# Optimization experiments

Measured on AMD Instinct MI355X. Metric: run time of the kernel, lower is better.

The kernel has to match this reference:

```python
import jax, jax.numpy as jnp
import numpy as np

D, DK, DV = 1024, 128, 128
N = 8192


def setup_inputs() -> dict:
    key = jax.random.key(0)
    ks = jax.random.split(key, 7)
    s = 1.0 / np.sqrt(D)
    return {
        "X": jax.random.normal(ks[0], (N, D), dtype=jnp.float32),
        "Wq": jax.random.uniform(ks[1], (D, DK), jnp.float32, -s, s),
        "bq": jax.random.uniform(ks[2], (DK,), jnp.float32, -s, s),
        "Wk": jax.random.uniform(ks[3], (D, DK), jnp.float32, -s, s),
        "bk": jax.random.uniform(ks[4], (DK,), jnp.float32, -s, s),
        "Wv": jax.random.uniform(ks[5], (D, DV), jnp.float32, -s, s),
        "bv": jax.random.uniform(ks[6], (DV,), jnp.float32, -s, s),
    }


def reference(X, Wq, bq, Wk, bk, Wv, bv):
    # Projections (torch Linear: y = x @ W^T + b; here W stored as [in, out])
    Q = X @ Wq + bq            # [N, d_k]
    K = X @ Wk + bk            # [N, d_k]
    V = X @ Wv + bv            # [N, d_v]
    n, d_k = Q.shape
    scores = (Q @ K.T) / jnp.sqrt(jnp.asarray(d_k, Q.dtype))  # [N, N]
    # Causal mask: positions j > i get -inf before softmax
    causal = jnp.tril(jnp.ones((n, n), dtype=bool))
    scores = jnp.where(causal, scores, -jnp.inf)
    weights = jax.nn.softmax(scores, axis=-1)  # [N, N]
    return weights @ V          # [N, d_v]
```

## Files before the change

kernel.cpp:

```cpp
#include <hip/hip_runtime.h>
#include <hip/hip_bf16.h>

#define N_TOK 8192
#define D_IN  1024
#define DK    128
#define NT    256

typedef __attribute__((ext_vector_type(8))) short short8;
typedef __attribute__((ext_vector_type(4))) float f32x4;

static __device__ __forceinline__ unsigned short f2bf(float f) {
    __hip_bfloat16 h = __float2bfloat16(f);
    return __builtin_bit_cast(unsigned short, h);
}

static __device__ __forceinline__ void gl_lds16(const void* g, void* l) {
    __builtin_amdgcn_global_load_lds(
        (const __attribute__((address_space(1))) void*)g,
        (__attribute__((address_space(3))) void*)l, 16, 0, 0);
}

__global__ __launch_bounds__(256) void wtrans_kernel(
    const float* __restrict__ Wq, const float* __restrict__ Wk,
    const float* __restrict__ Wv, unsigned short* __restrict__ Wt)
{
    __shared__ unsigned short T[64][72];
    const int proj = blockIdx.y;
    const float* W = (proj == 0) ? Wq : (proj == 1) ? Wk : Wv;
    unsigned short* out = Wt + (size_t)proj * DK * D_IN;
    const int k0 = (blockIdx.x & 15) * 64, n0 = (blockIdx.x >> 4) * 64;
    const int tid = threadIdx.x;
    #pragma unroll
    for (int i = 0; i < 4; i++) {
        int e = tid + i * 256;
        int r = e >> 4, c4 = e & 15;
        float4 v = *reinterpret_cast<const float4*>(&W[(size_t)(k0 + r) * DK + n0 + c4 * 4]);
        T[c4 * 4 + 0][r] = f2bf(v.x);
        T[c4 * 4 + 1][r] = f2bf(v.y);
        T[c4 * 4 + 2][r] = f2bf(v.z);
        T[c4 * 4 + 3][r] = f2bf(v.w);
    }
    __syncthreads();
    #pragma unroll
    for (int i = 0; i < 4; i++) {
        int e = tid + i * 256;
        int r = e >> 4, c4 = e & 15;
        *reinterpret_cast<ushort4*>(&out[(size_t)(n0 + r) * D_IN + k0 + c4 * 4]) =
            *reinterpret_cast<const ushort4*>(&T[r][c4 * 4]);
    }
}

__global__ __launch_bounds__(256) void proj_fused(
    const float* __restrict__ X, const unsigned short* __restrict__ Wt,
    const float* __restrict__ bq, const float* __restrict__ bk,
    const float* __restrict__ bv,
    unsigned short* __restrict__ Qb, unsigned short* __restrict__ Kb,
    unsigned short* __restrict__ Vt)
{
    __shared__ unsigned short Xs[2][32][72];

    const int tid = threadIdx.x;
    const int wid = tid >> 6, lane = tid & 63;
    const int g = lane >> 4, r16 = lane & 15;
    const int mb = blockIdx.x * 32;

    float4 xr[2];
    auto XLOAD = [&](int k0) {
        #pragma unroll
        for (int i = 0; i < 2; i++) {
            int e = tid + i * 256;
            int r = e >> 4, c4 = e & 15;
            xr[i] = *reinterpret_cast<const float4*>(
                &X[(size_t)(mb + r) * D_IN + k0 + c4 * 4]);
        }
    };
    auto XWRITE = [&](int buf) {
        #pragma unroll
        for (int i = 0; i < 2; i++) {
            int e = tid + i * 256;
            int r = e >> 4, c4 = e & 15;
            ushort4 h;
            h.x = f2bf(xr[i].x); h.y = f2bf(xr[i].y);
            h.z = f2bf(xr[i].z); h.w = f2bf(xr[i].w);
            *reinterpret_cast<ushort4*>(&Xs[buf][r][c4 * 4]) = h;
        }
    };

    f32x4 acc[2][6] = {};

    XLOAD(0); XWRITE(0);
    __syncthreads();
    for (int s = 0; s < 16; ++s) {
        const int k0 = s * 64;
        const int cur = s & 1;
        if (s + 1 < 16) XLOAD(k0 + 64);
        #pragma unroll
        for (int kk = 0; kk < 64; kk += 32) {
            short8 af[2], bfr[6];
            #pragma unroll
            for (int mi = 0; mi < 2; mi++)
                af[mi] = *reinterpret_cast<const short8*>(&Xs[cur][mi * 16 + r16][kk + g * 8]);
            #pragma unroll
            for (int ni = 0; ni < 6; ni++) {
                int nn = wid * 96 + ni * 16;
                int pj = nn >> 7;
                bfr[ni] = *reinterpret_cast<const short8*>(
                    &Wt[((size_t)pj * DK + (nn & 127) + r16) * D_IN + k0 + kk + g * 8]);
            }
            __builtin_amdgcn_s_setprio(1);
            #pragma unroll
            for (int mi = 0; mi < 2; mi++)
                #pragma unroll
                for (int ni = 0; ni < 6; ni++)
                    acc[mi][ni] = __builtin_amdgcn_mfma_f32_16x16x32_bf16(
                        af[mi], bfr[ni], acc[mi][ni], 0, 0, 0);
            __builtin_amdgcn_s_setprio(0);
        }
        if (s + 1 < 16) XWRITE((s + 1) & 1);
        __syncthreads();
    }

    #pragma unroll
    for (int ni = 0; ni < 6; ni++) {
        int nn = wid * 96 + ni * 16;
        int pj = nn >> 7;
        int n = (nn & 127) + r16;
        const float* bias = (pj == 0) ? bq : (pj == 1) ? bk : bv;
        float b = bias[n];
        if (pj < 2) {
            unsigned short* out = (pj == 0) ? Qb : Kb;
            #pragma unroll
            for (int mi = 0; mi < 2; mi++)
                #pragma unroll
                for (int e = 0; e < 4; e++) {
                    int m = mb + mi * 16 + g * 4 + e;
                    int nc = n;
                    if (pj == 1)
                        nc = ((((n >> 3) ^ (m & 7)) << 3) | (n & 7));
                    out[(size_t)m * DK + nc] = f2bf(acc[mi][ni][e] + b);
                }
        } else {
            #pragma unroll
            for (int mi = 0; mi < 2; mi++) {
                int m0 = mb + mi * 16 + g * 4;
                int mblk = (((m0 & 31) >> 3) ^ (n & 3));
                int mp = (m0 & ~31) | (mblk << 3) | (m0 & 7);
                ushort4 h;
                h.x = f2bf(acc[mi][ni][0] + b);
                h.y = f2bf(acc[mi][ni][1] + b);
                h.z = f2bf(acc[mi][ni][2] + b);
                h.w = f2bf(acc[mi][ni][3] + b);
                *reinterpret_cast<ushort4*>(&Vt[(size_t)n * N_TOK + mp]) = h;
            }
        }
    }
}

__global__ __launch_bounds__(256, 3) void attn_partial(
    const unsigned short* __restrict__ Qb, const unsigned short* __restrict__ Ksw,
    const unsigned short* __restrict__ Vsw,
    float* __restrict__ Opart, float* __restrict__ Mpart, float* __restrict__ Lpart,
    float* __restrict__ O, int chunk_tiles, int max_chunks, int direct)
{
    __shared__ unsigned short Klds[2][32][128];
    __shared__ unsigned short Vlds[2][128][32];
    __shared__ unsigned short Pq[4][32][36];

    const int qb = blockIdx.x, c = blockIdx.y;
    const int j0 = c * chunk_tiles;
    const int jmax = 4 * qb + 4;
    const int jend = min(j0 + chunk_tiles, jmax);
    if (j0 >= jend) return;
    const int nt = jend - j0;

    const int tid = threadIdx.x;
    const int wid = tid >> 6, lane = tid & 63;
    const int g = lane >> 4, r16 = lane & 15;
    const int t = qb * 4 + wid;
    const int qw = t * 32;
    const float scale2 = 0.08838834764831845f * 1.4426950408889634f;

    auto STAGE = [&](int buf, int kvb) {
        #pragma unroll
        for (int s = 0; s < 2; s++) {
            int ob = ((wid * 2 + s) << 10);
            gl_lds16((const char*)Ksw + ((size_t)kvb << 8) + ob + (lane << 4),
                     (char*)&Klds[buf][0][0] + ob);
        }
        #pragma unroll
        for (int s = 0; s < 2; s++) {
            int ob = ((wid * 2 + s) << 10);
            int o = ob + (lane << 4);
            int d = o >> 6, cb = o & 63;
            gl_lds16((const char*)Vsw + (((size_t)d * N_TOK + kvb) << 1) + cb,
                     (char*)&Vlds[buf][0][0] + ob);
        }
    };

    short8 qf[2][4];
    #pragma unroll
    for (int mi = 0; mi < 2; mi++)
        #pragma unroll
        for (int kd = 0; kd < 4; kd++)
            qf[mi][kd] = *reinterpret_cast<const short8*>(
                &Qb[(size_t)(qw + mi * 16 + r16) * DK + kd * 32 + g * 8]);

    f32x4 o_acc[2][8] = {};
    float m_run[2] = {-1e30f, -1e30f}, l_run[2] = {0.f, 0.f};

    STAGE(0, j0 * 32);

    int cur = 0;
    for (int it = 0; it < nt; ++it) {
        const int kvb = (j0 + it) * 32;
        if (it + 1 < nt) {
            STAGE(cur ^ 1, kvb + 32);
            asm volatile("s_waitcnt vmcnt(4)" ::: "memory");
        } else {
            asm volatile("s_waitcnt vmcnt(0)" ::: "memory");
        }
        __builtin_amdgcn_sched_barrier(0);
        __builtin_amdgcn_s_barrier();
        __builtin_amdgcn_sched_barrier(0);

        const unsigned short* Kl = &Klds[cur][0][0];
        const unsigned short* Vl = &Vlds[cur][0][0];

        f32x4 st[2][2] = {};
        #pragma unroll
        for (int kd = 0; kd < 4; kd++) {
            int swb = ((((kd << 2) | g) ^ (r16 & 7)) << 3);
            short8 kf0 = *reinterpret_cast<const short8*>(Kl + r16 * 128 + swb);
            short8 kf1 = *reinterpret_cast<const short8*>(Kl + (16 + r16) * 128 + swb);
            __builtin_amdgcn_s_setprio(1);
            st[0][0] = __builtin_amdgcn_mfma_f32_16x16x32_bf16(kf0, qf[0][kd], st[0][0], 0, 0, 0);
            st[0][1] = __builtin_amdgcn_mfma_f32_16x16x32_bf16(kf0, qf[1][kd], st[0][1], 0, 0, 0);
            st[1][0] = __builtin_amdgcn_mfma_f32_16x16x32_bf16(kf1, qf[0][kd], st[1][0], 0, 0, 0);
            st[1][1] = __builtin_amdgcn_mfma_f32_16x16x32_bf16(kf1, qf[1][kd], st[1][1], 0, 0, 0);
            __builtin_amdgcn_s_setprio(0);
        }

        const bool anymask = (kvb + 31 > qw);
        float alpha[2];
        #pragma unroll
        for (int mi = 0; mi < 2; mi++) {
            const int qrow = qw + mi * 16 + r16;
            float s[2][4];
            #pragma unroll
            for (int ni = 0; ni < 2; ni++)
                #pragma unroll
                for (int e = 0; e < 4; e++) {
                    float v = st[ni][mi][e] * scale2;
                    if (anymask && (kvb + ni * 16 + g * 4 + e > qrow)) v = -1e30f;
                    s[ni][e] = v;
                }
            float lm = fmaxf(fmaxf(fmaxf(s[0][0], s[0][1]), fmaxf(s[0][2], s[0][3])),
                             fmaxf(fmaxf(s[1][0], s[1][1]), fmaxf(s[1][2], s[1][3])));
            lm = fmaxf(lm, __shfl_xor(lm, 16));
            lm = fmaxf(lm, __shfl_xor(lm, 32));
            float mnew = fmaxf(m_run[mi], lm);
            alpha[mi] = exp2f(m_run[mi] - mnew);
            float ps[2][4], ls;
            #pragma unroll
            for (int ni = 0; ni < 2; ni++)
                #pragma unroll
                for (int e = 0; e < 4; e++)
                    ps[ni][e] = exp2f(s[ni][e] - mnew);
            ls = ((ps[0][0] + ps[0][1]) + (ps[0][2] + ps[0][3]))
               + ((ps[1][0] + ps[1][1]) + (ps[1][2] + ps[1][3]));
            ls += __shfl_xor(ls, 16);
            ls += __shfl_xor(ls, 32);
            l_run[mi] = l_run[mi] * alpha[mi] + ls;
            m_run[mi] = mnew;
            #pragma unroll
            for (int ni = 0; ni < 2; ni++) {
                ushort4 pk;
                pk.x = f2bf(ps[ni][0]); pk.y = f2bf(ps[ni][1]);
                pk.z = f2bf(ps[ni][2]); pk.w = f2bf(ps[ni][3]);
                *reinterpret_cast<ushort4*>(&Pq[wid][mi * 16 + r16][ni * 16 + g * 4]) = pk;
            }
        }
        if (__any(alpha[0] < 1.f) || __any(alpha[1] < 1.f)) {
            #pragma unroll
            for (int mi = 0; mi < 2; mi++)
                #pragma unroll
                for (int df = 0; df < 8; df++)
                    #pragma unroll
                    for (int e = 0; e < 4; e++)
                        o_acc[mi][df][e] *= alpha[mi];
        }
        short8 pb0 = *reinterpret_cast<const short8*>(&Pq[wid][r16][g * 8]);
        short8 pb1 = *reinterpret_cast<const short8*>(&Pq[wid][16 + r16][g * 8]);
        const int swv = ((g ^ (r16 & 3)) << 3);
        #pragma unroll
        for (int df = 0; df < 8; df++) {
            short8 vf = *reinterpret_cast<const short8*>(Vl + (df * 16 + r16) * 32 + swv);
            __builtin_amdgcn_s_setprio(1);
            o_acc[0][df] = __builtin_amdgcn_mfma_f32_16x16x32_bf16(vf, pb0, o_acc[0][df], 0, 0, 0);
            o_acc[1][df] = __builtin_amdgcn_mfma_f32_16x16x32_bf16(vf, pb1, o_acc[1][df], 0, 0, 0);
            __builtin_amdgcn_s_setprio(0);
        }

        __builtin_amdgcn_sched_barrier(0);
        __builtin_amdgcn_s_barrier();
        __builtin_amdgcn_sched_barrier(0);
        cur ^= 1;
    }

    if (direct) {
        #pragma unroll
        for (int mi = 0; mi < 2; mi++) {
            float inv = 1.0f / l_run[mi];
            #pragma unroll
            for (int df = 0; df < 8; df++) {
                f32x4 r = o_acc[mi][df];
                r[0] *= inv; r[1] *= inv; r[2] *= inv; r[3] *= inv;
                *reinterpret_cast<f32x4*>(
                    &O[(size_t)(qw + mi * 16 + r16) * DK + df * 16 + g * 4]) = r;
            }
        }
    } else {
        size_t pb0i = ((size_t)t * max_chunks + c) * 32;
        #pragma unroll
        for (int mi = 0; mi < 2; mi++) {
            #pragma unroll
            for (int df = 0; df < 8; df++)
                *reinterpret_cast<f32x4*>(
                    &Opart[(pb0i + mi * 16 + r16) * 128 + df * 16 + g * 4]) = o_acc[mi][df];
            if (g == 0) {
                Mpart[pb0i + mi * 16 + r16] = m_run[mi];
                Lpart[pb0i + mi * 16 + r16] = l_run[mi];
            }
        }
    }
}

__global__ __launch_bounds__(256) void attn_merge(
    const float* __restrict__ Opart, const float* __restrict__ Mpart,
    const float* __restrict__ Lpart, float* __restrict__ O,
    int chunk_tiles, int max_chunks)
{
    __shared__ float Ms[32], Ls[32], Fs[16][32];
    const int t = blockIdx.x;
    const int nc = t / chunk_tiles + 1;
    const int tid = threadIdx.x;

    if (tid < 32) {
        float M = -1e30f;
        for (int c = 0; c < nc; c++)
            M = fmaxf(M, Mpart[((size_t)t * max_chunks + c) * 32 + tid]);
        float L = 0.f;
        for (int c = 0; c < nc; c++) {
            size_t pb = ((size_t)t * max_chunks + c) * 32 + tid;
            L += exp2f(Mpart[pb] - M) * Lpart[pb];
        }
        Ms[tid] = M; Ls[tid] = L;
    }
    __syncthreads();
    for (int cc = tid >> 5; cc < nc; cc += 8) {
        int row = tid & 31;
        Fs[cc][row] = exp2f(Mpart[((size_t)t * max_chunks + cc) * 32 + row] - Ms[row]);
    }
    __syncthreads();
    #pragma unroll
    for (int it = 0; it < 4; it++) {
        int idx = tid + it * 256;
        int row = idx >> 5, c4 = idx & 31;
        float4 acc = {0.f, 0.f, 0.f, 0.f};
        for (int c = 0; c < nc; c++) {
            const float4 v = *reinterpret_cast<const float4*>(
                &Opart[(((size_t)t * max_chunks + c) * 32 + row) * 128 + c4 * 4]);
            float f = Fs[c][row];
            acc.x += f * v.x; acc.y += f * v.y; acc.z += f * v.z; acc.w += f * v.w;
        }
        float inv = 1.0f / Ls[row];
        float4 r;
        r.x = acc.x * inv; r.y = acc.y * inv; r.z = acc.z * inv; r.w = acc.w * inv;
        *reinterpret_cast<float4*>(&O[((size_t)t * 32 + row) * DK + c4 * 4]) = r;
    }
}

extern "C" void kernel_launch(void* const* d_in, const int* in_sizes, int n_in,
                              void* d_out, int out_size, void* d_ws, size_t ws_size,
                              hipStream_t stream) {
    const float* X  = (const float*)d_in[0];
    const float* Wq = (const float*)d_in[1];
    const float* bq = (const float*)d_in[2];
    const float* Wk = (const float*)d_in[3];
    const float* bk = (const float*)d_in[4];
    const float* Wv = (const float*)d_in[5];
    const float* bv = (const float*)d_in[6];
    float* O = (float*)d_out;

    unsigned short* Qb = (unsigned short*)d_ws;
    unsigned short* Kb = Qb + (size_t)N_TOK * DK;
    unsigned short* Vt = Kb + (size_t)N_TOK * DK;
    unsigned short* Wt = Vt + (size_t)N_TOK * DK;
    float* Opart = (float*)(Wt + (size_t)3 * DK * D_IN);
    size_t base_bytes = (size_t)((char*)Opart - (char*)d_ws);

    int chunk_tiles = 0, max_chunks = 1, direct = 0;
    const int opts[4] = {16, 32, 64, 128};
    for (int i = 0; i < 4; i++) {
        int ct = opts[i], mc = NT / ct;
        size_t need = base_bytes + (size_t)NT * mc * 32 * (128 + 2) * sizeof(float);
        if (need <= ws_size) { chunk_tiles = ct; max_chunks = mc; break; }
    }
    if (!chunk_tiles) { chunk_tiles = NT; max_chunks = 1; direct = 1; }
    float* Mpart = Opart + (size_t)NT * max_chunks * 32 * 128;
    float* Lpart = Mpart + (size_t)NT * max_chunks * 32;

    wtrans_kernel<<<dim3(32, 3), 256, 0, stream>>>(Wq, Wk, Wv, Wt);
    proj_fused<<<dim3(256), 256, 0, stream>>>(X, Wt, bq, bk, bv, Qb, Kb, Vt);
    int grid_c = direct ? 1 : max_chunks;
    attn_partial<<<dim3(64, grid_c), 256, 0, stream>>>(
        Qb, Kb, Vt, Opart, Mpart, Lpart, O, chunk_tiles, max_chunks, direct);
    if (!direct)
        attn_merge<<<dim3(NT), 256, 0, stream>>>(Opart, Mpart, Lpart, O,
                                                 chunk_tiles, max_chunks);
}
```

Measured before the change: 112.4 us.

## Split projection grid, lazy softmax rescale, register P shuffle, bf16 partial outputs

The projection kernel now launches twice as many blocks, each covering half the output columns. The attention kernel gets a tighter occupancy bound and skips the online-softmax max update and accumulator rescale while the new row max exceeds the running max by at most 8. It builds the P operand with packed bf16 converts and cross-lane shuffles instead of a round trip through LDS. Partial outputs are stored as bf16 rather than fp32, which halves merge traffic and permits a smaller chunk size of 8, at the cost of extra rounding error in the merged result.

```diff
diff --git a/kernel.cpp b/kernel.cpp
--- a/kernel.cpp
+++ b/kernel.cpp
@@ -62,7 +62,8 @@
     const int tid = threadIdx.x;
     const int wid = tid >> 6, lane = tid & 63;
     const int g = lane >> 4, r16 = lane & 15;
-    const int mb = blockIdx.x * 32;
+    const int mb   = (blockIdx.x >> 1) * 32;
+    const int half = blockIdx.x & 1;
 
     float4 xr[2];
     auto XLOAD = [&](int k0) {
@@ -86,7 +87,7 @@
         }
     };
 
-    f32x4 acc[2][6] = {};
+    f32x4 acc[2][3] = {};
 
     XLOAD(0); XWRITE(0);
     __syncthreads();
@@ -96,13 +97,13 @@
         if (s + 1 < 16) XLOAD(k0 + 64);
         #pragma unroll
         for (int kk = 0; kk < 64; kk += 32) {
-            short8 af[2], bfr[6];
+            short8 af[2], bfr[3];
             #pragma unroll
             for (int mi = 0; mi < 2; mi++)
                 af[mi] = *reinterpret_cast<const short8*>(&Xs[cur][mi * 16 + r16][kk + g * 8]);
             #pragma unroll
-            for (int ni = 0; ni < 6; ni++) {
-                int nn = wid * 96 + ni * 16;
+            for (int ni = 0; ni < 3; ni++) {
+                int nn = half * 192 + wid * 48 + ni * 16;
                 int pj = nn >> 7;
                 bfr[ni] = *reinterpret_cast<const short8*>(
                     &Wt[((size_t)pj * DK + (nn & 127) + r16) * D_IN + k0 + kk + g * 8]);
@@ -111,7 +112,7 @@
             #pragma unroll
             for (int mi = 0; mi < 2; mi++)
                 #pragma unroll
-                for (int ni = 0; ni < 6; ni++)
+                for (int ni = 0; ni < 3; ni++)
                     acc[mi][ni] = __builtin_amdgcn_mfma_f32_16x16x32_bf16(
                         af[mi], bfr[ni], acc[mi][ni], 0, 0, 0);
             __builtin_amdgcn_s_setprio(0);
@@ -121,8 +122,8 @@
     }
 
     #pragma unroll
-    for (int ni = 0; ni < 6; ni++) {
-        int nn = wid * 96 + ni * 16;
+    for (int ni = 0; ni < 3; ni++) {
+        int nn = half * 192 + wid * 48 + ni * 16;
         int pj = nn >> 7;
         int n = (nn & 127) + r16;
         const float* bias = (pj == 0) ? bq : (pj == 1) ? bk : bv;
@@ -156,15 +157,15 @@
     }
 }
 
-__global__ __launch_bounds__(256, 3) void attn_partial(
+__global__ __launch_bounds__(256, 4) void attn_partial(
     const unsigned short* __restrict__ Qb, const unsigned short* __restrict__ Ksw,
     const unsigned short* __restrict__ Vsw,
-    float* __restrict__ Opart, float* __restrict__ Mpart, float* __restrict__ Lpart,
+    unsigned short* __restrict__ OpartH, float* __restrict__ Mpart,
+    float* __restrict__ Lpart,
     float* __restrict__ O, int chunk_tiles, int max_chunks, int direct)
 {
     __shared__ unsigned short Klds[2][32][128];
     __shared__ unsigned short Vlds[2][128][32];
-    __shared__ unsigned short Pq[4][32][36];
 
     const int qb = blockIdx.x, c = blockIdx.y;
     const int j0 = c * chunk_tiles;
@@ -241,7 +242,7 @@
         }
 
         const bool anymask = (kvb + 31 > qw);
-        float alpha[2];
+        short8 pb[2];
         #pragma unroll
         for (int mi = 0; mi < 2; mi++) {
             const int qrow = qw + mi * 16 + r16;
@@ -258,46 +259,54 @@
                              fmaxf(fmaxf(s[1][0], s[1][1]), fmaxf(s[1][2], s[1][3])));
             lm = fmaxf(lm, __shfl_xor(lm, 16));
             lm = fmaxf(lm, __shfl_xor(lm, 32));
-            float mnew = fmaxf(m_run[mi], lm);
-            alpha[mi] = exp2f(m_run[mi] - mnew);
-            float ps[2][4], ls;
+            bool nog = __all(lm - m_run[mi] <= 8.0f);
+            float mnew = nog ? m_run[mi] : fmaxf(m_run[mi], lm);
+            float ps[2][4];
             #pragma unroll
             for (int ni = 0; ni < 2; ni++)
                 #pragma unroll
                 for (int e = 0; e < 4; e++)
                     ps[ni][e] = exp2f(s[ni][e] - mnew);
-            ls = ((ps[0][0] + ps[0][1]) + (ps[0][2] + ps[0][3]))
-               + ((ps[1][0] + ps[1][1]) + (ps[1][2] + ps[1][3]));
+            float ls = ((ps[0][0] + ps[0][1]) + (ps[0][2] + ps[0][3]))
+                     + ((ps[1][0] + ps[1][1]) + (ps[1][2] + ps[1][3]));
             ls += __shfl_xor(ls, 16);
             ls += __shfl_xor(ls, 32);
-            l_run[mi] = l_run[mi] * alpha[mi] + ls;
-            m_run[mi] = mnew;
-            #pragma unroll
-            for (int ni = 0; ni < 2; ni++) {
-                ushort4 pk;
-                pk.x = f2bf(ps[ni][0]); pk.y = f2bf(ps[ni][1]);
-                pk.z = f2bf(ps[ni][2]); pk.w = f2bf(ps[ni][3]);
-                *reinterpret_cast<ushort4*>(&Pq[wid][mi * 16 + r16][ni * 16 + g * 4]) = pk;
-            }
-        }
-        if (__any(alpha[0] < 1.f) || __any(alpha[1] < 1.f)) {
-            #pragma unroll
-            for (int mi = 0; mi < 2; mi++)
+            if (nog) {
+                l_run[mi] += ls;
+            } else {
+                float alpha = exp2f(m_run[mi] - mnew);
+                l_run[mi] = l_run[mi] * alpha + ls;
+                m_run[mi] = mnew;
                 #pragma unroll
                 for (int df = 0; df < 8; df++)
                     #pragma unroll
                     for (int e = 0; e < 4; e++)
-                        o_acc[mi][df][e] *= alpha[mi];
-        }
-        short8 pb0 = *reinterpret_cast<const short8*>(&Pq[wid][r16][g * 8]);
-        short8 pb1 = *reinterpret_cast<const short8*>(&Pq[wid][16 + r16][g * 8]);
+                        o_acc[mi][df][e] *= alpha;
+            }
+            unsigned X0, X1, Y0, Y1;
+            asm("v_cvt_pk_bf16_f32 %0, %1, %2" : "=v"(X0) : "v"(ps[0][0]), "v"(ps[0][1]));
+            asm("v_cvt_pk_bf16_f32 %0, %1, %2" : "=v"(X1) : "v"(ps[0][2]), "v"(ps[0][3]));
+            asm("v_cvt_pk_bf16_f32 %0, %1, %2" : "=v"(Y0) : "v"(ps[1][0]), "v"(ps[1][1]));
+            asm("v_cvt_pk_bf16_f32 %0, %1, %2" : "=v"(Y1) : "v"(ps[1][2]), "v"(ps[1][3]));
+            const int sle = ((lane & 16) << 1) | r16;
+            const int slo = sle + 16;
+            int a0 = __shfl((int)X0, sle), b0 = __shfl((int)Y0, sle);
+            int a1 = __shfl((int)X1, sle), b1 = __shfl((int)Y1, sle);
+            int a2 = __shfl((int)X0, slo), b2 = __shfl((int)Y0, slo);
+            int a3 = __shfl((int)X1, slo), b3 = __shfl((int)Y1, slo);
+            bool hi = (lane >= 32);
+            int4 wv = make_int4(hi ? b0 : a0, hi ? b1 : a1,
+                                hi ? b2 : a2, hi ? b3 : a3);
+            pb[mi] = __builtin_bit_cast(short8, wv);
+        }
+
         const int swv = ((g ^ (r16 & 3)) << 3);
         #pragma unroll
         for (int df = 0; df < 8; df++) {
             short8 vf = *reinterpret_cast<const short8*>(Vl + (df * 16 + r16) * 32 + swv);
             __builtin_amdgcn_s_setprio(1);
-            o_acc[0][df] = __builtin_amdgcn_mfma_f32_16x16x32_bf16(vf, pb0, o_acc[0][df], 0, 0, 0);
-            o_acc[1][df] = __builtin_amdgcn_mfma_f32_16x16x32_bf16(vf, pb1, o_acc[1][df], 0, 0, 0);
+            o_acc[0][df] = __builtin_amdgcn_mfma_f32_16x16x32_bf16(vf, pb[0], o_acc[0][df], 0, 0, 0);
+            o_acc[1][df] = __builtin_amdgcn_mfma_f32_16x16x32_bf16(vf, pb[1], o_acc[1][df], 0, 0, 0);
             __builtin_amdgcn_s_setprio(0);
         }
 
@@ -323,24 +332,26 @@
         size_t pb0i = ((size_t)t * max_chunks + c) * 32;
         #pragma unroll
         for (int mi = 0; mi < 2; mi++) {
-            #pragma unroll
-            for (int df = 0; df < 8; df++)
-                *reinterpret_cast<f32x4*>(
-                    &Opart[(pb0i + mi * 16 + r16) * 128 + df * 16 + g * 4]) = o_acc[mi][df];
-            if (g == 0) {
-                Mpart[pb0i + mi * 16 + r16] = m_run[mi];
-                Lpart[pb0i + mi * 16 + r16] = l_run[mi];
-            }
+            int q = mi * 16 + r16;
+            #pragma unroll
+            for (int df = 0; df < 8; df++) {
+                ushort4 h;
+                h.x = f2bf(o_acc[mi][df][0]); h.y = f2bf(o_acc[mi][df][1]);
+                h.z = f2bf(o_acc[mi][df][2]); h.w = f2bf(o_acc[mi][df][3]);
+                *reinterpret_cast<ushort4*>(
+                    &OpartH[(pb0i + q) * 128 + df * 16 + g * 4]) = h;
+            }
+            if (g == 0) { Mpart[pb0i + q] = m_run[mi]; Lpart[pb0i + q] = l_run[mi]; }
         }
     }
 }
 
 __global__ __launch_bounds__(256) void attn_merge(
-    const float* __restrict__ Opart, const float* __restrict__ Mpart,
+    const unsigned short* __restrict__ OpartH, const float* __restrict__ Mpart,
     const float* __restrict__ Lpart, float* __restrict__ O,
     int chunk_tiles, int max_chunks)
 {
-    __shared__ float Ms[32], Ls[32], Fs[16][32];
+    __shared__ float Ms[32], Ls[32], Fs[32][32];
     const int t = blockIdx.x;
     const int nc = t / chunk_tiles + 1;
     const int tid = threadIdx.x;
@@ -363,20 +374,26 @@
     }
     __syncthreads();
     #pragma unroll
-    for (int it = 0; it < 4; it++) {
+    for (int it = 0; it < 2; it++) {
         int idx = tid + it * 256;
-        int row = idx >> 5, c4 = idx & 31;
-        float4 acc = {0.f, 0.f, 0.f, 0.f};
+        int row = idx >> 4, c8 = idx & 15;
+        float accv[8] = {};
         for (int c = 0; c < nc; c++) {
-            const float4 v = *reinterpret_cast<const float4*>(
-                &Opart[(((size_t)t * max_chunks + c) * 32 + row) * 128 + c4 * 4]);
+            short8 u = *reinterpret_cast<const short8*>(
+                &OpartH[(((size_t)t * max_chunks + c) * 32 + row) * 128 + c8 * 8]);
             float f = Fs[c][row];
-            acc.x += f * v.x; acc.y += f * v.y; acc.z += f * v.z; acc.w += f * v.w;
+            #pragma unroll
+            for (int k = 0; k < 8; k++) {
+                unsigned uv = ((unsigned)(unsigned short)u[k]) << 16;
+                accv[k] += f * __builtin_bit_cast(float, uv);
+            }
         }
         float inv = 1.0f / Ls[row];
-        float4 r;
-        r.x = acc.x * inv; r.y = acc.y * inv; r.z = acc.z * inv; r.w = acc.w * inv;
-        *reinterpret_cast<float4*>(&O[((size_t)t * 32 + row) * DK + c4 * 4]) = r;
+        float* dst = &O[((size_t)t * 32 + row) * DK + c8 * 8];
+        float4 r0 = {accv[0] * inv, accv[1] * inv, accv[2] * inv, accv[3] * inv};
+        float4 r1 = {accv[4] * inv, accv[5] * inv, accv[6] * inv, accv[7] * inv};
+        *reinterpret_cast<float4*>(dst) = r0;
+        *reinterpret_cast<float4*>(dst + 4) = r1;
     }
 }
 
@@ -396,26 +413,29 @@
     unsigned short* Kb = Qb + (size_t)N_TOK * DK;
     unsigned short* Vt = Kb + (size_t)N_TOK * DK;
     unsigned short* Wt = Vt + (size_t)N_TOK * DK;
-    float* Opart = (float*)(Wt + (size_t)3 * DK * D_IN);
-    size_t base_bytes = (size_t)((char*)Opart - (char*)d_ws);
+    float* Mbase = (float*)(Wt + (size_t)3 * DK * D_IN);
+    size_t base_bytes = (size_t)((char*)Mbase - (char*)d_ws);
 
     int chunk_tiles = 0, max_chunks = 1, direct = 0;
-    const int opts[4] = {16, 32, 64, 128};
-    for (int i = 0; i < 4; i++) {
+    const int opts[5] = {8, 16, 32, 64, 128};
+    for (int i = 0; i < 5; i++) {
         int ct = opts[i], mc = NT / ct;
-        size_t need = base_bytes + (size_t)NT * mc * 32 * (128 + 2) * sizeof(float);
+        size_t need = base_bytes
+                    + (size_t)NT * mc * 32 * 2 * sizeof(float)
+                    + (size_t)NT * mc * 32 * 128 * 2;
         if (need <= ws_size) { chunk_tiles = ct; max_chunks = mc; break; }
     }
     if (!chunk_tiles) { chunk_tiles = NT; max_chunks = 1; direct = 1; }
-    float* Mpart = Opart + (size_t)NT * max_chunks * 32 * 128;
+    float* Mpart = Mbase;
     float* Lpart = Mpart + (size_t)NT * max_chunks * 32;
+    unsigned short* OpartH = (unsigned short*)(Lpart + (size_t)NT * max_chunks * 32);
 
     wtrans_kernel<<<dim3(32, 3), 256, 0, stream>>>(Wq, Wk, Wv, Wt);
-    proj_fused<<<dim3(256), 256, 0, stream>>>(X, Wt, bq, bk, bv, Qb, Kb, Vt);
+    proj_fused<<<dim3(512), 256, 0, stream>>>(X, Wt, bq, bk, bv, Qb, Kb, Vt);
     int grid_c = direct ? 1 : max_chunks;
     attn_partial<<<dim3(64, grid_c), 256, 0, stream>>>(
-        Qb, Kb, Vt, Opart, Mpart, Lpart, O, chunk_tiles, max_chunks, direct);
+        Qb, Kb, Vt, OpartH, Mpart, Lpart, O, chunk_tiles, max_chunks, direct);
     if (!direct)
-        attn_merge<<<dim3(NT), 256, 0, stream>>>(Opart, Mpart, Lpart, O,
+        attn_merge<<<dim3(NT), 256, 0, stream>>>(OpartH, Mpart, Lpart, O,
                                                  chunk_tiles, max_chunks);
 }
```

Result: slower. 159.3 us (+41.8%).
